# Performance work log

Hardware: AMD Instinct MI355X
Metric: run time of the kernel (lower is better)

The kernel has to match this reference:

```python
import jax, jax.numpy as jnp
import numpy as np


def setup_inputs() -> dict:
    key = jax.random.key(0)
    k0, k1, k2, k3, k4 = jax.random.split(key, 5)
    B, F, E = 16384, 39, 64
    R = max(1, F // 3)  # reduction_ratio = 3 -> 13
    return {
        "inputs": jax.random.normal(k0, (B, F, E), dtype=jnp.float32),
        "W_1": jax.random.normal(k1, (F, R), dtype=jnp.float32) * (2.0 / (F + R)) ** 0.5,
        "W_2": jax.random.normal(k2, (R, F), dtype=jnp.float32) * (2.0 / (F + R)) ** 0.5,
        "W_3": jax.random.normal(k3, (F, R), dtype=jnp.float32) * (2.0 / (F + R)) ** 0.5,
        "W_4": jax.random.normal(k4, (R, F), dtype=jnp.float32) * (2.0 / (F + R)) ** 0.5,
    }


def reference(inputs, W_1, W_2, W_3, W_4):
    # inputs: [B, F, E] (fields already concatenated along axis=1)
    # --- SE-style gating branch ---
    Z = jnp.mean(inputs, axis=-1)                       # [B, F]
    A_2 = jax.nn.relu(jax.nn.relu(Z @ W_1) @ W_2)       # [B, F]
    V = inputs * A_2[:, :, None]                        # [B, F, E]
    # --- soft-threshold branch ---
    inputs_abs = jnp.abs(inputs)
    abs_mean = jnp.mean(inputs_abs, axis=-1)            # [B, F]
    A_2_ = jax.nn.relu(jax.nn.relu(abs_mean @ W_3) @ W_4)  # [B, F]
    thres = (abs_mean * A_2_)[:, :, None]               # [B, F, 1]
    n_sub = jnp.maximum(inputs_abs - thres, 0.0)        # soft threshold magnitude
    R = jnp.sign(inputs) * n_sub                        # [B, F, E]
    # concat on embedding axis; original then splits into F [B,1,2E] slices
    return jnp.concatenate([V, R], axis=-1)             # [B, F, 2E]
```

## Files before the change

kernel.cpp:

```cpp
#include <hip/hip_runtime.h>


#define SEST_B 16384
#define SEST_F 39
#define SEST_E 64
#define SEST_R 13

__global__ __launch_bounds__(256) void sest_kernel(
    const float* __restrict__ x,
    const float* __restrict__ W1,
    const float* __restrict__ W2,
    const float* __restrict__ W3,
    const float* __restrict__ W4,
    float* __restrict__ out)
{
    const int b    = blockIdx.x;
    const int tid  = threadIdx.x;
    const int w    = tid >> 6;
    const int lane = tid & 63;
    const int g    = lane >> 4;
    const int s    = lane & 15;

    __shared__ float Zm[SEST_F];
    __shared__ float Am[SEST_F];
    __shared__ float H1[SEST_R];
    __shared__ float H2[SEST_R];
    __shared__ float A2s[SEST_F];
    __shared__ float Th[SEST_F];

    const float4* in4 = reinterpret_cast<const float4*>(x)
                        + (size_t)b * SEST_F * (SEST_E / 4);

    float4 xr[3];
    #pragma unroll
    for (int i = 0; i < 3; ++i) {
        const int f = i * 16 + w * 4 + g;
        float sx = 0.f, sa = 0.f;
        if (f < SEST_F) {
            float4 v = in4[f * (SEST_E / 4) + s];
            xr[i] = v;
            sx = v.x + v.y + v.z + v.w;
            sa = fabsf(v.x) + fabsf(v.y) + fabsf(v.z) + fabsf(v.w);
        }
        #pragma unroll
        for (int m = 1; m < 16; m <<= 1) {
            sx += __shfl_xor(sx, m);
            sa += __shfl_xor(sa, m);
        }
        if (f < SEST_F && s == 0) {
            Zm[f] = sx * (1.0f / 64.0f);
            Am[f] = sa * (1.0f / 64.0f);
        }
    }
    __syncthreads();

    if (tid < SEST_R) {
        float acc = 0.f;
        #pragma unroll
        for (int f = 0; f < SEST_F; ++f) acc += Zm[f] * W1[f * SEST_R + tid];
        H1[tid] = fmaxf(acc, 0.f);
    } else if (tid >= 64 && tid < 64 + SEST_R) {
        const int r = tid - 64;
        float acc = 0.f;
        #pragma unroll
        for (int f = 0; f < SEST_F; ++f) acc += Am[f] * W3[f * SEST_R + r];
        H2[r] = fmaxf(acc, 0.f);
    }
    __syncthreads();

    if (tid < SEST_F) {
        float acc = 0.f;
        #pragma unroll
        for (int r = 0; r < SEST_R; ++r) acc += H1[r] * W2[r * SEST_F + tid];
        A2s[tid] = fmaxf(acc, 0.f);
    } else if (tid >= 64 && tid < 64 + SEST_F) {
        const int f = tid - 64;
        float acc = 0.f;
        #pragma unroll
        for (int r = 0; r < SEST_R; ++r) acc += H2[r] * W4[r * SEST_F + f];
        Th[f] = Am[f] * fmaxf(acc, 0.f);
    }
    __syncthreads();

    float4* out4 = reinterpret_cast<float4*>(out)
                   + (size_t)b * SEST_F * (2 * SEST_E / 4);
    #pragma unroll
    for (int i = 0; i < 3; ++i) {
        const int f = i * 16 + w * 4 + g;
        if (f < SEST_F) {
            const float a2 = A2s[f];
            const float th = Th[f];
            const float4 v = xr[i];
            float4 V, R;
            V.x = v.x * a2; V.y = v.y * a2; V.z = v.z * a2; V.w = v.w * a2;
            R.x = copysignf(fmaxf(fabsf(v.x) - th, 0.f), v.x);
            R.y = copysignf(fmaxf(fabsf(v.y) - th, 0.f), v.y);
            R.z = copysignf(fmaxf(fabsf(v.z) - th, 0.f), v.z);
            R.w = copysignf(fmaxf(fabsf(v.w) - th, 0.f), v.w);
            out4[f * 32 + s]      = V;
            out4[f * 32 + 16 + s] = R;
        }
    }
}

extern "C" void kernel_launch(void* const* d_in, const int* in_sizes, int n_in,
                              void* d_out, int out_size, void* d_ws, size_t ws_size,
                              hipStream_t stream) {
    const float* x  = (const float*)d_in[0];
    const float* W1 = (const float*)d_in[1];
    const float* W2 = (const float*)d_in[2];
    const float* W3 = (const float*)d_in[3];
    const float* W4 = (const float*)d_in[4];
    float* out = (float*)d_out;

    sest_kernel<<<SEST_B, 256, 0, stream>>>(x, W1, W2, W3, W4, out);
}
```

Baseline: 446.9 us.

## Map one wavefront per batch row with shuffle-based MLP and shared weights

Each 64-lane wavefront now handles one batch row instead of a whole 256-thread block doing so, with four rows per block. The SE/threshold MLPs are computed with warp shuffles and no per-row block barriers, and the weights are staged once per block in shared memory. This is meant to remove the three __syncthreads per row and the serial single-thread matvec phases that left most threads idle. In exchange each thread holds 10 float4 values in registers, and a launch bound requesting 4 blocks per multiprocessor may constrain register allocation.

```diff
diff --git a/kernel.cpp b/kernel.cpp
--- a/kernel.cpp
+++ b/kernel.cpp
@@ -5,8 +5,9 @@
 #define SEST_F 39
 #define SEST_E 64
 #define SEST_R 13
+#define WPB    4
 
-__global__ __launch_bounds__(256) void sest_kernel(
+__global__ __launch_bounds__(256, 4) void sest_kernel(
     const float* __restrict__ x,
     const float* __restrict__ W1,
     const float* __restrict__ W2,
@@ -14,30 +15,35 @@
     const float* __restrict__ W4,
     float* __restrict__ out)
 {
-    const int b    = blockIdx.x;
     const int tid  = threadIdx.x;
     const int w    = tid >> 6;
     const int lane = tid & 63;
     const int g    = lane >> 4;
     const int s    = lane & 15;
+    const int b    = blockIdx.x * WPB + w;
 
-    __shared__ float Zm[SEST_F];
-    __shared__ float Am[SEST_F];
-    __shared__ float H1[SEST_R];
-    __shared__ float H2[SEST_R];
-    __shared__ float A2s[SEST_F];
-    __shared__ float Th[SEST_F];
+    __shared__ float sW1[SEST_F * SEST_R];
+    __shared__ float sW2[SEST_R * SEST_F];
+    __shared__ float sW3[SEST_F * SEST_R];
+    __shared__ float sW4[SEST_R * SEST_F];
+    for (int i = tid; i < SEST_F * SEST_R; i += 256) {
+        sW1[i] = W1[i];
+        sW2[i] = W2[i];
+        sW3[i] = W3[i];
+        sW4[i] = W4[i];
+    }
 
     const float4* in4 = reinterpret_cast<const float4*>(x)
-                        + (size_t)b * SEST_F * (SEST_E / 4);
+                        + (size_t)b * (SEST_F * (SEST_E / 4));
 
-    float4 xr[3];
+    float4 xr[10];
+    float  zm[10], am[10];
     #pragma unroll
-    for (int i = 0; i < 3; ++i) {
-        const int f = i * 16 + w * 4 + g;
+    for (int i = 0; i < 10; ++i) {
+        const int f = i * 4 + g;
         float sx = 0.f, sa = 0.f;
         if (f < SEST_F) {
-            float4 v = in4[f * (SEST_E / 4) + s];
+            const float4 v = in4[f * (SEST_E / 4) + s];
             xr[i] = v;
             sx = v.x + v.y + v.z + v.w;
             sa = fabsf(v.x) + fabsf(v.y) + fabsf(v.z) + fabsf(v.w);
@@ -47,58 +53,54 @@
             sx += __shfl_xor(sx, m);
             sa += __shfl_xor(sa, m);
         }
-        if (f < SEST_F && s == 0) {
-            Zm[f] = sx * (1.0f / 64.0f);
-            Am[f] = sa * (1.0f / 64.0f);
-        }
+        zm[i] = sx * (1.0f / 64.0f);
+        am[i] = sa * (1.0f / 64.0f);
     }
+
     __syncthreads();
 
-    if (tid < SEST_R) {
-        float acc = 0.f;
-        #pragma unroll
-        for (int f = 0; f < SEST_F; ++f) acc += Zm[f] * W1[f * SEST_R + tid];
-        H1[tid] = fmaxf(acc, 0.f);
-    } else if (tid >= 64 && tid < 64 + SEST_R) {
-        const int r = tid - 64;
-        float acc = 0.f;
-        #pragma unroll
-        for (int f = 0; f < SEST_F; ++f) acc += Am[f] * W3[f * SEST_R + r];
-        H2[r] = fmaxf(acc, 0.f);
+    const int rl = lane & 15;
+    const int rc = (rl < SEST_R) ? rl : 0;
+    float acc1 = 0.f, acc3 = 0.f;
+    #pragma unroll
+    for (int f = 0; f < SEST_F; ++f) {
+        const float zf = __shfl(zm[f >> 2], (f & 3) << 4);
+        const float af = __shfl(am[f >> 2], (f & 3) << 4);
+        acc1 = fmaf(zf, sW1[f * SEST_R + rc], acc1);
+        acc3 = fmaf(af, sW3[f * SEST_R + rc], acc3);
     }
-    __syncthreads();
+    const float h1 = fmaxf(acc1, 0.f);
+    const float h2 = fmaxf(acc3, 0.f);
 
-    if (tid < SEST_F) {
-        float acc = 0.f;
-        #pragma unroll
-        for (int r = 0; r < SEST_R; ++r) acc += H1[r] * W2[r * SEST_F + tid];
-        A2s[tid] = fmaxf(acc, 0.f);
-    } else if (tid >= 64 && tid < 64 + SEST_F) {
-        const int f = tid - 64;
-        float acc = 0.f;
-        #pragma unroll
-        for (int r = 0; r < SEST_R; ++r) acc += H2[r] * W4[r * SEST_F + f];
-        Th[f] = Am[f] * fmaxf(acc, 0.f);
+    const int fc = (lane < SEST_F) ? lane : 0;
+    float acc2 = 0.f, acc4 = 0.f;
+    #pragma unroll
+    for (int r = 0; r < SEST_R; ++r) {
+        const float h1r = __shfl(h1, r);
+        const float h2r = __shfl(h2, r);
+        acc2 = fmaf(h1r, sW2[r * SEST_F + fc], acc2);
+        acc4 = fmaf(h2r, sW4[r * SEST_F + fc], acc4);
     }
-    __syncthreads();
+    const float a2v = fmaxf(acc2, 0.f);
+    const float thv = fmaxf(acc4, 0.f);
 
     float4* out4 = reinterpret_cast<float4*>(out)
-                   + (size_t)b * SEST_F * (2 * SEST_E / 4);
+                   + (size_t)b * (SEST_F * (2 * SEST_E / 4));
     #pragma unroll
-    for (int i = 0; i < 3; ++i) {
-        const int f = i * 16 + w * 4 + g;
+    for (int i = 0; i < 10; ++i) {
+        const int f  = i * 4 + g;
+        const float a2 = __shfl(a2v, f);
+        const float th = am[i] * __shfl(thv, f);
         if (f < SEST_F) {
-            const float a2 = A2s[f];
-            const float th = Th[f];
             const float4 v = xr[i];
-            float4 V, R;
+            float4 V, Rv;
             V.x = v.x * a2; V.y = v.y * a2; V.z = v.z * a2; V.w = v.w * a2;
-            R.x = copysignf(fmaxf(fabsf(v.x) - th, 0.f), v.x);
-            R.y = copysignf(fmaxf(fabsf(v.y) - th, 0.f), v.y);
-            R.z = copysignf(fmaxf(fabsf(v.z) - th, 0.f), v.z);
-            R.w = copysignf(fmaxf(fabsf(v.w) - th, 0.f), v.w);
+            Rv.x = copysignf(fmaxf(fabsf(v.x) - th, 0.f), v.x);
+            Rv.y = copysignf(fmaxf(fabsf(v.y) - th, 0.f), v.y);
+            Rv.z = copysignf(fmaxf(fabsf(v.z) - th, 0.f), v.z);
+            Rv.w = copysignf(fmaxf(fabsf(v.w) - th, 0.f), v.w);
             out4[f * 32 + s]      = V;
-            out4[f * 32 + 16 + s] = R;
+            out4[f * 32 + 16 + s] = Rv;
         }
     }
 }
@@ -113,5 +115,5 @@
     const float* W4 = (const float*)d_in[4];
     float* out = (float*)d_out;
 
-    sest_kernel<<<SEST_B, 256, 0, stream>>>(x, W1, W2, W3, W4, out);
+    sest_kernel<<<SEST_B / WPB, 256, 0, stream>>>(x, W1, W2, W3, W4, out);
 }
```

Result: no change. 445.1 us (-0.4%).
